# Kernel tuning notes

Measured on AMD Instinct MI355X. Metric: run time of the kernel, lower is better.

The kernel has to match this reference:

```python
import jax, jax.numpy as jnp
import numpy as np

K = 128      # knowledge_n (= net1 = prednet output width)
LOW = 64     # low_dim
PP = 64      # pp_dim
STU = 50000  # student_n
EXER = 20000 # exer_n
S_RANGES = [(0, 9999), (10000, 19999)]
NR = len(S_RANGES)
B = 4096


def setup_inputs() -> dict:
    key = jax.random.key(0)
    ks = jax.random.split(key, 16)

    def xavier(k, shape):
        fan_in, fan_out = shape[-1], shape[-2] if len(shape) > 1 else shape[-1]
        lim = np.sqrt(6.0 / (fan_in + fan_out))
        return jax.random.uniform(k, shape, jnp.float32, -lim, lim)

    return {
        "stu_id": jax.random.randint(ks[0], (B,), 0, STU),
        "exer_id": jax.random.randint(ks[1], (B,), 0, EXER),
        "kn_emb": jnp.ones((B, K), jnp.float32),
        "student_emb": xavier(ks[2], (NR, STU, LOW)),          # ParameterList stacked
        "prompt_stu": xavier(ks[3], (STU, PP)),
        "knowledge_emb": jax.random.normal(ks[4], (K, LOW), jnp.float32),
        "k_difficulty": xavier(ks[5], (EXER, LOW)),
        "s_exer_vectors": jax.random.uniform(ks[6], (NR, PP), jnp.float32),
        "W1": xavier(ks[7], (K, K + LOW)),                      # prednet_full1 (no bias)
        "W2": xavier(ks[8], (K, K + LOW)),                      # prednet_full2 (no bias)
        "W3": xavier(ks[9], (1, K)),                            # prednet_full3
        "b3": jnp.zeros((1,), jnp.float32),
        "fc1_W": xavier(ks[10], (K, PP + K)),
        "fc1_b": jnp.zeros((K,), jnp.float32),
        "fc2_W": xavier(ks[11], (K, PP + K)),
        "fc2_b": jnp.zeros((K,), jnp.float32),
    }


def reference(stu_id, exer_id, kn_emb, student_emb, prompt_stu, knowledge_emb,
              k_difficulty, s_exer_vectors, W1, W2, W3, b3, fc1_W, fc1_b, fc2_W, fc2_b):
    sig = jax.nn.sigmoid
    kle = knowledge_emb  # [K, LOW]

    # --- student side ---
    # prompt_stu.repeat(NR, 1) then index_select == index prompt_stu with stu_id % STU
    p_stu = prompt_stu[stu_id % STU]                              # [B, PP]
    stu_cat = student_emb.reshape(NR * STU, LOW)                  # concat of ParameterList
    old_stu = sig(stu_cat[stu_id] @ kle.T)                        # [B, K]
    stu_e = sig(jnp.concatenate([p_stu, old_stu], 1) @ fc1_W.T + fc1_b)  # [B, K]

    # --- exercise side ---
    counts = np.array([r[1] - r[0] + 1 for r in S_RANGES])
    temp_vectors = jnp.repeat(s_exer_vectors, counts, axis=0, total_repeat_length=EXER)
    p_exer = sig(temp_vectors[exer_id])                           # [B, PP]
    old_exer = sig(sig(k_difficulty[exer_id]) @ kle.T)            # [B, K]
    exer_e = sig(jnp.concatenate([p_exer, old_exer], 1) @ fc2_W.T + fc2_b)  # [B, K]

    # --- per-concept interaction ---
    # cat([x_broadcast, kn_vector], 2) @ W.T splits into x @ Wa.T + kle @ Wb.T
    W1a, W1b = W1[:, :K], W1[:, K:]
    W2a, W2b = W2[:, :K], W2[:, K:]
    preference = sig((stu_e @ W1a.T)[:, None, :] + (kle @ W1b.T)[None, :, :])   # [B, K, K]
    diff = sig((exer_e @ W2a.T)[:, None, :] + (kle @ W2b.T)[None, :, :])        # [B, K, K]

    o = sig((preference - diff) @ W3.T + b3)                      # [B, K, 1]
    sum_out = jnp.sum(o * kn_emb[:, :, None], axis=1)             # [B, 1]
    count = jnp.sum(kn_emb, axis=1, keepdims=True)
    return sum_out / count
```

## Files before the change

kernel.cpp:

```cpp
#include <hip/hip_runtime.h>
#include <hip/hip_bf16.h>

#define STUN   50000
#define BATCH  4096
#define LOG2E  1.4426950408889634f

__device__ __forceinline__ float fexp2(float x){ return __builtin_amdgcn_exp2f(x); }
__device__ __forceinline__ float frcp (float x){ return __builtin_amdgcn_rcpf(x); }
__device__ __forceinline__ float fsig (float x){ return frcp(1.0f + fexp2(-LOG2E * x)); }

__global__ __launch_bounds__(128) void k_pre(
    const float* __restrict__ kle,
    const float* __restrict__ W1,
    const float* __restrict__ W2,
    const float* __restrict__ fc1_W,
    const float* __restrict__ fc2_W,
    float* __restrict__ kleT,
    float* __restrict__ fc1T,
    float* __restrict__ fc2T,
    float* __restrict__ W1aT,
    float* __restrict__ W2aT,
    float* __restrict__ E1i,
    float* __restrict__ E2i)
{
    const int bid = blockIdx.x;
    const int t   = threadIdx.x;
    if (bid < 64) {
        const int u = bid;
        kleT[u * 128 + t] = kle[t * 64 + u];
    } else if (bid < 256) {
        const int u = bid - 64;
        fc1T[u * 128 + t] = fc1_W[t * 192 + u];
    } else if (bid < 448) {
        const int u = bid - 256;
        fc2T[u * 128 + t] = fc2_W[t * 192 + u];
    } else if (bid < 576) {
        const int u = bid - 448;
        W1aT[u * 128 + t] = W1[t * 192 + u];
    } else if (bid < 704) {
        const int u = bid - 576;
        W2aT[u * 128 + t] = W2[t * 192 + u];
    } else if (bid < 832) {
        const int j = bid - 704;
        float acc = 0.f;
        #pragma unroll
        for (int u4 = 0; u4 < 16; ++u4) {
            const float4 kv = *(const float4*)&kle[t * 64 + u4 * 4];
            const float4 wv = *(const float4*)&W1[j * 192 + 128 + u4 * 4];
            acc += kv.x * wv.x + kv.y * wv.y + kv.z * wv.z + kv.w * wv.w;
        }
        E1i[((j >> 2) * 128 + t) * 4 + (j & 3)] = fexp2(-LOG2E * acc);
    } else {
        const int j = bid - 832;
        float acc = 0.f;
        #pragma unroll
        for (int u4 = 0; u4 < 16; ++u4) {
            const float4 kv = *(const float4*)&kle[t * 64 + u4 * 4];
            const float4 wv = *(const float4*)&W2[j * 192 + 128 + u4 * 4];
            acc += kv.x * wv.x + kv.y * wv.y + kv.z * wv.z + kv.w * wv.w;
        }
        E2i[((j >> 2) * 128 + t) * 4 + (j & 3)] = fexp2(-LOG2E * acc);
    }
}

__global__ __launch_bounds__(256, 4) void k_fused(
    const int*   __restrict__ stu_id,
    const int*   __restrict__ exer_id,
    const float* __restrict__ student_emb,
    const float* __restrict__ prompt_stu,
    const float* __restrict__ k_diff,
    const float* __restrict__ s_exer,
    const float* __restrict__ kleT,
    const float* __restrict__ fc1T,
    const float* __restrict__ fc2T,
    const float* __restrict__ W1aT,
    const float* __restrict__ W2aT,
    const float* __restrict__ fc1_b,
    const float* __restrict__ fc2_b,
    const float* __restrict__ E1i,
    const float* __restrict__ E2i,
    const float* __restrict__ W3,
    const float* __restrict__ b3,
    const float* __restrict__ kn,
    float* __restrict__ out)
{
    __shared__ __align__(16) float sh_in [4][64][4];
    __shared__ __align__(16) float sh_old[2][128][4];
    __shared__ __align__(16) float sh_e  [2][128][4];
    __shared__ __align__(16) float ps[4][2][32][20];
    __shared__ __align__(16) float ses[2][4][128];
    __shared__ float r_o[4][2];
    __shared__ float r_k[4][2];

    const int t  = threadIdx.x;
    const int b0 = blockIdx.x * 4;

    {
        const int g   = t >> 6;
        const int u   = t & 63;
        const int sid = stu_id[b0 + g];
        const int eid = exer_id[b0 + g];
        const int er  = (eid >= 10000) ? 1 : 0;
        sh_in[0][u][g] = student_emb[sid * 64 + u];
        sh_in[1][u][g] = fsig(k_diff[eid * 64 + u]);
        sh_in[2][u][g] = prompt_stu[(sid % STUN) * 64 + u];
        sh_in[3][u][g] = fsig(s_exer[er * 64 + u]);
    }
    __syncthreads();

    const int wv   = t >> 6;
    const int l    = t & 63;
    const int half = l >> 5;
    const int iq   = l & 31;
    float* myps = &ps[wv][half][iq][0];

    const int ch   = t >> 7;
    const int cidx = t & 127;
    const int ciq  = cidx >> 2;
    const int cc   = cidx & 3;

    float a[4][4];

#define CLR { _Pragma("unroll") for (int c = 0; c < 4; ++c) \
              _Pragma("unroll") for (int b = 0; b < 4; ++b) a[c][b] = 0.f; }

#define FMAC(c, wc) { \
    a[c][0] = fmaf(wc, x0.x, a[c][0]); a[c][1] = fmaf(wc, x0.y, a[c][1]); \
    a[c][2] = fmaf(wc, x0.z, a[c][2]); a[c][3] = fmaf(wc, x0.w, a[c][3]); }

#define GSTEP(wp, xp) { \
    const float4 w4 = *(const float4*)(wp); \
    const float4 x0 = *(const float4*)&(xp)[0]; \
    FMAC(0, w4.x); FMAC(1, w4.y); FMAC(2, w4.z); FMAC(3, w4.w); }

#define PSTORE { _Pragma("unroll") for (int b = 0; b < 4; ++b) \
    *(float4*)&myps[b * 4] = make_float4(a[0][b], a[1][b], a[2][b], a[3][b]); }

#define PCOMB(res) float res[4]; \
    _Pragma("unroll") for (int b = 0; b < 4; ++b) \
        res[b] = ps[0][ch][ciq][b * 4 + cc] + ps[1][ch][ciq][b * 4 + cc] \
               + ps[2][ch][ciq][b * 4 + cc] + ps[3][ch][ciq][b * 4 + cc];

    CLR;
    {
        const int u0 = wv * 16;
        #pragma unroll 4
        for (int u = u0; u < u0 + 16; ++u)
            GSTEP(&kleT[u * 128 + iq * 4], sh_in[half][u]);
    }
    PSTORE;
    __syncthreads();
    {
        PCOMB(s);
        #pragma unroll
        for (int b = 0; b < 4; ++b) sh_old[ch][cidx][b] = fsig(s[b]);
    }
    __syncthreads();

    CLR;
    {
        const float* fcT = half ? fc2T : fc1T;
        const int u0 = wv * 48;
        const int ue_in = (u0 + 48 < 64) ? u0 + 48 : 64;
        #pragma unroll 4
        for (int u = u0; u < ue_in; ++u)
            GSTEP(&fcT[u * 128 + iq * 4], sh_in[2 + half][u]);
        const int us_old = (u0 > 64) ? u0 : 64;
        #pragma unroll 4
        for (int u = us_old; u < u0 + 48; ++u)
            GSTEP(&fcT[u * 128 + iq * 4], sh_old[half][u - 64]);
    }
    PSTORE;
    __syncthreads();
    {
        PCOMB(s);
        const float bias = (ch ? fc2_b : fc1_b)[cidx];
        #pragma unroll
        for (int b = 0; b < 4; ++b) sh_e[ch][cidx][b] = fsig(s[b] + bias);
    }
    __syncthreads();

    CLR;
    {
        const float* WT = half ? W2aT : W1aT;
        const int u0 = wv * 32;
        #pragma unroll 4
        for (int u = u0; u < u0 + 32; ++u)
            GSTEP(&WT[u * 128 + iq * 4], sh_e[half][u]);
    }
    PSTORE;
    __syncthreads();
    {
        PCOMB(s);
        #pragma unroll
        for (int b = 0; b < 4; ++b)
            ses[ch][b][cidx] = fexp2(-LOG2E * s[b]);
    }
#undef CLR
#undef FMAC
#undef GSTEP
#undef PSTORE
#undef PCOMB
    __syncthreads();

    const int k  = t & 127;
    const int bh = t >> 7;
    const int i0 = bh * 2;

    const float4* E1v = (const float4*)E1i + k;
    const float4* E2v = (const float4*)E2i + k;

    float acc0 = 0.f, acc1 = 0.f;

#define COMP(acc, esv1, esv2, e1c, e2c, w3c) { \
        const float uu = (esv1) * (e1c); \
        const float vv = (esv2) * (e2c); \
        const float dd = frcp((1.f + uu) * (1.f + vv)); \
        acc = fmaf((vv - uu) * dd, (w3c), acc); }

    #pragma unroll 4
    for (int j4 = 0; j4 < 32; ++j4) {
        const int j = j4 * 4;
        const float4 e1  = E1v[j4 * 128];
        const float4 e2  = E2v[j4 * 128];
        const float4 w3  = *(const float4*)&W3[j];
        const float4 p1a = *(const float4*)&ses[0][i0 + 0][j];
        const float4 p2a = *(const float4*)&ses[1][i0 + 0][j];
        const float4 p1b = *(const float4*)&ses[0][i0 + 1][j];
        const float4 p2b = *(const float4*)&ses[1][i0 + 1][j];
        COMP(acc0, p1a.x, p2a.x, e1.x, e2.x, w3.x);
        COMP(acc0, p1a.y, p2a.y, e1.y, e2.y, w3.y);
        COMP(acc0, p1a.z, p2a.z, e1.z, e2.z, w3.z);
        COMP(acc0, p1a.w, p2a.w, e1.w, e2.w, w3.w);
        COMP(acc1, p1b.x, p2b.x, e1.x, e2.x, w3.x);
        COMP(acc1, p1b.y, p2b.y, e1.y, e2.y, w3.y);
        COMP(acc1, p1b.z, p2b.z, e1.z, e2.z, w3.z);
        COMP(acc1, p1b.w, p2b.w, e1.w, e2.w, w3.w);
    }
#undef COMP

    const float bb3 = b3[0];
    const float o0  = fsig(acc0 + bb3);
    const float o1  = fsig(acc1 + bb3);
    const float kn0 = kn[(b0 + i0 + 0) * 128 + k];
    const float kn1 = kn[(b0 + i0 + 1) * 128 + k];
    float co0 = o0 * kn0, ck0 = kn0;
    float co1 = o1 * kn1, ck1 = kn1;
    #pragma unroll
    for (int off = 1; off < 64; off <<= 1) {
        co0 += __shfl_xor(co0, off);
        ck0 += __shfl_xor(ck0, off);
        co1 += __shfl_xor(co1, off);
        ck1 += __shfl_xor(ck1, off);
    }
    const int w = t >> 6;
    if ((t & 63) == 0) {
        r_o[w][0] = co0; r_o[w][1] = co1;
        r_k[w][0] = ck0; r_k[w][1] = ck1;
    }
    __syncthreads();
    if (t < 4) {
        const int bhh = t >> 1;
        const int i   = t & 1;
        const float so = r_o[bhh * 2][i] + r_o[bhh * 2 + 1][i];
        const float sk = r_k[bhh * 2][i] + r_k[bhh * 2 + 1][i];
        out[b0 + bhh * 2 + i] = so / sk;
    }
}

extern "C" void kernel_launch(void* const* d_in, const int* in_sizes, int n_in,
                              void* d_out, int out_size, void* d_ws, size_t ws_size,
                              hipStream_t stream)
{
    const int*   stu_id      = (const int*)  d_in[0];
    const int*   exer_id     = (const int*)  d_in[1];
    const float* kn_emb      = (const float*)d_in[2];
    const float* student_emb = (const float*)d_in[3];
    const float* prompt_stu  = (const float*)d_in[4];
    const float* kle         = (const float*)d_in[5];
    const float* k_diff      = (const float*)d_in[6];
    const float* s_exer      = (const float*)d_in[7];
    const float* W1          = (const float*)d_in[8];
    const float* W2          = (const float*)d_in[9];
    const float* W3          = (const float*)d_in[10];
    const float* b3          = (const float*)d_in[11];
    const float* fc1_W       = (const float*)d_in[12];
    const float* fc1_b       = (const float*)d_in[13];
    const float* fc2_W       = (const float*)d_in[14];
    const float* fc2_b       = (const float*)d_in[15];
    float* out = (float*)d_out;

    float* ws   = (float*)d_ws;
    float* kleT = ws;
    float* fc1T = kleT + 8192;
    float* fc2T = fc1T + 24576;
    float* W1aT = fc2T + 24576;
    float* W2aT = W1aT + 16384;
    float* E1i  = W2aT + 16384;
    float* E2i  = E1i  + 16384;

    k_pre  <<<960, 128, 0, stream>>>(kle, W1, W2, fc1_W, fc2_W,
                                     kleT, fc1T, fc2T, W1aT, W2aT, E1i, E2i);
    k_fused<<<BATCH / 4, 256, 0, stream>>>(stu_id, exer_id, student_emb, prompt_stu,
                                           k_diff, s_exer, kleT, fc1T, fc2T,
                                           W1aT, W2aT, fc1_b, fc2_b,
                                           E1i, E2i, W3, b3, kn_emb, out);
}
```

Measured before the change: 46.41 us.

## Double fused block to 512 threads and reduce GEMV partials with wave shuffles

```diff
diff --git a/kernel.cpp b/kernel.cpp
--- a/kernel.cpp
+++ b/kernel.cpp
@@ -63,7 +63,7 @@
     }
 }
 
-__global__ __launch_bounds__(256, 4) void k_fused(
+__global__ __launch_bounds__(512, 4) void k_fused(
     const int*   __restrict__ stu_id,
     const int*   __restrict__ exer_id,
     const float* __restrict__ student_emb,
@@ -87,184 +87,169 @@
     __shared__ __align__(16) float sh_in [4][64][4];
     __shared__ __align__(16) float sh_old[2][128][4];
     __shared__ __align__(16) float sh_e  [2][128][4];
-    __shared__ __align__(16) float ps[4][2][32][20];
-    __shared__ __align__(16) float ses[2][4][128];
-    __shared__ float r_o[4][2];
-    __shared__ float r_k[4][2];
+    __shared__ __align__(16) float ses   [2][4][128];
+    __shared__ float red_o[8];
+    __shared__ float red_k[8];
 
     const int t  = threadIdx.x;
     const int b0 = blockIdx.x * 4;
 
     {
-        const int g   = t >> 6;
+        const int g   = t >> 7;
+        const int sp  = (t >> 6) & 1;
         const int u   = t & 63;
         const int sid = stu_id[b0 + g];
         const int eid = exer_id[b0 + g];
-        const int er  = (eid >= 10000) ? 1 : 0;
-        sh_in[0][u][g] = student_emb[sid * 64 + u];
-        sh_in[1][u][g] = fsig(k_diff[eid * 64 + u]);
-        sh_in[2][u][g] = prompt_stu[(sid % STUN) * 64 + u];
-        sh_in[3][u][g] = fsig(s_exer[er * 64 + u]);
-    }
-    __syncthreads();
-
-    const int wv   = t >> 6;
+        if (sp == 0) {
+            sh_in[0][u][g] = student_emb[sid * 64 + u];
+            sh_in[1][u][g] = fsig(k_diff[eid * 64 + u]);
+        } else {
+            const int er = (eid >= 10000) ? 1 : 0;
+            sh_in[2][u][g] = prompt_stu[(sid % STUN) * 64 + u];
+            sh_in[3][u][g] = fsig(s_exer[er * 64 + u]);
+        }
+    }
+    __syncthreads();
+
+    const int w    = t >> 6;
+    const int half = w & 1;
+    const int iqo  = w >> 1;
     const int l    = t & 63;
-    const int half = l >> 5;
-    const int iq   = l & 31;
-    float* myps = &ps[wv][half][iq][0];
-
-    const int ch   = t >> 7;
-    const int cidx = t & 127;
-    const int ciq  = cidx >> 2;
-    const int cc   = cidx & 3;
-
-    float a[4][4];
-
-#define CLR { _Pragma("unroll") for (int c = 0; c < 4; ++c) \
-              _Pragma("unroll") for (int b = 0; b < 4; ++b) a[c][b] = 0.f; }
-
-#define FMAC(c, wc) { \
-    a[c][0] = fmaf(wc, x0.x, a[c][0]); a[c][1] = fmaf(wc, x0.y, a[c][1]); \
-    a[c][2] = fmaf(wc, x0.z, a[c][2]); a[c][3] = fmaf(wc, x0.w, a[c][3]); }
-
-#define GSTEP(wp, xp) { \
+    const int ul   = l >> 4;
+    const int bh2  = (l >> 3) & 1;
+    const int iql  = l & 7;
+    const int iq   = iqo * 8 + iql;
+
+    float a[4][2];
+
+#define CLR { _Pragma("unroll") for (int c = 0; c < 4; ++c) { a[c][0] = 0.f; a[c][1] = 0.f; } }
+
+#define GSTEP2(wp, xp) { \
     const float4 w4 = *(const float4*)(wp); \
-    const float4 x0 = *(const float4*)&(xp)[0]; \
-    FMAC(0, w4.x); FMAC(1, w4.y); FMAC(2, w4.z); FMAC(3, w4.w); }
-
-#define PSTORE { _Pragma("unroll") for (int b = 0; b < 4; ++b) \
-    *(float4*)&myps[b * 4] = make_float4(a[0][b], a[1][b], a[2][b], a[3][b]); }
-
-#define PCOMB(res) float res[4]; \
-    _Pragma("unroll") for (int b = 0; b < 4; ++b) \
-        res[b] = ps[0][ch][ciq][b * 4 + cc] + ps[1][ch][ciq][b * 4 + cc] \
-               + ps[2][ch][ciq][b * 4 + cc] + ps[3][ch][ciq][b * 4 + cc];
+    const float2 x2 = *(const float2*)(xp); \
+    a[0][0] = fmaf(w4.x, x2.x, a[0][0]); a[0][1] = fmaf(w4.x, x2.y, a[0][1]); \
+    a[1][0] = fmaf(w4.y, x2.x, a[1][0]); a[1][1] = fmaf(w4.y, x2.y, a[1][1]); \
+    a[2][0] = fmaf(w4.z, x2.x, a[2][0]); a[2][1] = fmaf(w4.z, x2.y, a[2][1]); \
+    a[3][0] = fmaf(w4.w, x2.x, a[3][0]); a[3][1] = fmaf(w4.w, x2.y, a[3][1]); }
+
+#define COMBINE { _Pragma("unroll") for (int c = 0; c < 4; ++c) { \
+    _Pragma("unroll") for (int b = 0; b < 2; ++b) { \
+        float v = a[c][b]; \
+        v += __shfl_xor(v, 16); \
+        v += __shfl_xor(v, 32); \
+        a[c][b] = v; } } }
 
     CLR;
     {
-        const int u0 = wv * 16;
-        #pragma unroll 4
+        const int u0 = ul * 16;
+        #pragma unroll
         for (int u = u0; u < u0 + 16; ++u)
-            GSTEP(&kleT[u * 128 + iq * 4], sh_in[half][u]);
-    }
-    PSTORE;
-    __syncthreads();
-    {
-        PCOMB(s);
-        #pragma unroll
-        for (int b = 0; b < 4; ++b) sh_old[ch][cidx][b] = fsig(s[b]);
+            GSTEP2(&kleT[u * 128 + iq * 4], &sh_in[half][u][bh2 * 2]);
+    }
+    COMBINE;
+    if (ul == 0) {
+        #pragma unroll
+        for (int c = 0; c < 4; ++c) {
+            const float2 v2 = make_float2(fsig(a[c][0]), fsig(a[c][1]));
+            *(float2*)&sh_old[half][iq * 4 + c][bh2 * 2] = v2;
+        }
     }
     __syncthreads();
 
     CLR;
     {
         const float* fcT = half ? fc2T : fc1T;
-        const int u0 = wv * 48;
-        const int ue_in = (u0 + 48 < 64) ? u0 + 48 : 64;
-        #pragma unroll 4
-        for (int u = u0; u < ue_in; ++u)
-            GSTEP(&fcT[u * 128 + iq * 4], sh_in[2 + half][u]);
-        const int us_old = (u0 > 64) ? u0 : 64;
-        #pragma unroll 4
-        for (int u = us_old; u < u0 + 48; ++u)
-            GSTEP(&fcT[u * 128 + iq * 4], sh_old[half][u - 64]);
-    }
-    PSTORE;
-    __syncthreads();
-    {
-        PCOMB(s);
-        const float bias = (ch ? fc2_b : fc1_b)[cidx];
-        #pragma unroll
-        for (int b = 0; b < 4; ++b) sh_e[ch][cidx][b] = fsig(s[b] + bias);
+        const int up = ul * 16;
+        #pragma unroll
+        for (int u = up; u < up + 16; ++u)
+            GSTEP2(&fcT[u * 128 + iq * 4], &sh_in[2 + half][u][bh2 * 2]);
+        const int uo = ul * 32;
+        #pragma unroll
+        for (int u = uo; u < uo + 32; ++u)
+            GSTEP2(&fcT[(64 + u) * 128 + iq * 4], &sh_old[half][u][bh2 * 2]);
+    }
+    COMBINE;
+    if (ul == 0) {
+        const float* fcb = half ? fc2_b : fc1_b;
+        #pragma unroll
+        for (int c = 0; c < 4; ++c) {
+            const float bias = fcb[iq * 4 + c];
+            const float2 v2 = make_float2(fsig(a[c][0] + bias), fsig(a[c][1] + bias));
+            *(float2*)&sh_e[half][iq * 4 + c][bh2 * 2] = v2;
+        }
     }
     __syncthreads();
 
     CLR;
     {
         const float* WT = half ? W2aT : W1aT;
-        const int u0 = wv * 32;
-        #pragma unroll 4
+        const int u0 = ul * 32;
+        #pragma unroll
         for (int u = u0; u < u0 + 32; ++u)
-            GSTEP(&WT[u * 128 + iq * 4], sh_e[half][u]);
-    }
-    PSTORE;
-    __syncthreads();
-    {
-        PCOMB(s);
-        #pragma unroll
-        for (int b = 0; b < 4; ++b)
-            ses[ch][b][cidx] = fexp2(-LOG2E * s[b]);
+            GSTEP2(&WT[u * 128 + iq * 4], &sh_e[half][u][bh2 * 2]);
+    }
+    COMBINE;
+    if (ul == 0) {
+        #pragma unroll
+        for (int c = 0; c < 4; ++c) {
+            ses[half][bh2 * 2 + 0][iq * 4 + c] = fexp2(-LOG2E * a[c][0]);
+            ses[half][bh2 * 2 + 1][iq * 4 + c] = fexp2(-LOG2E * a[c][1]);
+        }
     }
 #undef CLR
-#undef FMAC
-#undef GSTEP
-#undef PSTORE
-#undef PCOMB
+#undef GSTEP2
+#undef COMBINE
     __syncthreads();
 
     const int k  = t & 127;
     const int bh = t >> 7;
-    const int i0 = bh * 2;
 
     const float4* E1v = (const float4*)E1i + k;
     const float4* E2v = (const float4*)E2i + k;
-
-    float acc0 = 0.f, acc1 = 0.f;
-
-#define COMP(acc, esv1, esv2, e1c, e2c, w3c) { \
-        const float uu = (esv1) * (e1c); \
-        const float vv = (esv2) * (e2c); \
+    const float* s1 = &ses[0][bh][0];
+    const float* s2 = &ses[1][bh][0];
+
+    float acc = 0.f;
+
+#define COMP(s1c, s2c, e1c, e2c, w3c) { \
+        const float uu = (s1c) * (e1c); \
+        const float vv = (s2c) * (e2c); \
         const float dd = frcp((1.f + uu) * (1.f + vv)); \
         acc = fmaf((vv - uu) * dd, (w3c), acc); }
 
     #pragma unroll 4
     for (int j4 = 0; j4 < 32; ++j4) {
         const int j = j4 * 4;
-        const float4 e1  = E1v[j4 * 128];
-        const float4 e2  = E2v[j4 * 128];
-        const float4 w3  = *(const float4*)&W3[j];
-        const float4 p1a = *(const float4*)&ses[0][i0 + 0][j];
-        const float4 p2a = *(const float4*)&ses[1][i0 + 0][j];
-        const float4 p1b = *(const float4*)&ses[0][i0 + 1][j];
-        const float4 p2b = *(const float4*)&ses[1][i0 + 1][j];
-        COMP(acc0, p1a.x, p2a.x, e1.x, e2.x, w3.x);
-        COMP(acc0, p1a.y, p2a.y, e1.y, e2.y, w3.y);
-        COMP(acc0, p1a.z, p2a.z, e1.z, e2.z, w3.z);
-        COMP(acc0, p1a.w, p2a.w, e1.w, e2.w, w3.w);
-        COMP(acc1, p1b.x, p2b.x, e1.x, e2.x, w3.x);
-        COMP(acc1, p1b.y, p2b.y, e1.y, e2.y, w3.y);
-        COMP(acc1, p1b.z, p2b.z, e1.z, e2.z, w3.z);
-        COMP(acc1, p1b.w, p2b.w, e1.w, e2.w, w3.w);
+        const float4 e1 = E1v[j4 * 128];
+        const float4 e2 = E2v[j4 * 128];
+        const float4 w3 = *(const float4*)&W3[j];
+        const float4 p1 = *(const float4*)&s1[j];
+        const float4 p2 = *(const float4*)&s2[j];
+        COMP(p1.x, p2.x, e1.x, e2.x, w3.x);
+        COMP(p1.y, p2.y, e1.y, e2.y, w3.y);
+        COMP(p1.z, p2.z, e1.z, e2.z, w3.z);
+        COMP(p1.w, p2.w, e1.w, e2.w, w3.w);
     }
 #undef COMP
 
     const float bb3 = b3[0];
-    const float o0  = fsig(acc0 + bb3);
-    const float o1  = fsig(acc1 + bb3);
-    const float kn0 = kn[(b0 + i0 + 0) * 128 + k];
-    const float kn1 = kn[(b0 + i0 + 1) * 128 + k];
-    float co0 = o0 * kn0, ck0 = kn0;
-    float co1 = o1 * kn1, ck1 = kn1;
+    const float o   = fsig(acc + bb3);
+    const float knv = kn[(b0 + bh) * 128 + k];
+    float co = o * knv, ck = knv;
     #pragma unroll
     for (int off = 1; off < 64; off <<= 1) {
-        co0 += __shfl_xor(co0, off);
-        ck0 += __shfl_xor(ck0, off);
-        co1 += __shfl_xor(co1, off);
-        ck1 += __shfl_xor(ck1, off);
-    }
-    const int w = t >> 6;
+        co += __shfl_xor(co, off);
+        ck += __shfl_xor(ck, off);
+    }
     if ((t & 63) == 0) {
-        r_o[w][0] = co0; r_o[w][1] = co1;
-        r_k[w][0] = ck0; r_k[w][1] = ck1;
+        red_o[w] = co;
+        red_k[w] = ck;
     }
     __syncthreads();
     if (t < 4) {
-        const int bhh = t >> 1;
-        const int i   = t & 1;
-        const float so = r_o[bhh * 2][i] + r_o[bhh * 2 + 1][i];
-        const float sk = r_k[bhh * 2][i] + r_k[bhh * 2 + 1][i];
-        out[b0 + bhh * 2 + i] = so / sk;
+        const float so = red_o[2 * t] + red_o[2 * t + 1];
+        const float sk = red_k[2 * t] + red_k[2 * t + 1];
+        out[b0 + t] = so / sk;
     }
 }
 
@@ -301,7 +286,7 @@
 
     k_pre  <<<960, 128, 0, stream>>>(kle, W1, W2, fc1_W, fc2_W,
                                      kleT, fc1T, fc2T, W1aT, W2aT, E1i, E2i);
-    k_fused<<<BATCH / 4, 256, 0, stream>>>(stu_id, exer_id, student_emb, prompt_stu,
+    k_fused<<<BATCH / 4, 512, 0, stream>>>(stu_id, exer_id, student_emb, prompt_stu,
                                            k_diff, s_exer, kleT, fc1T, fc2T,
                                            W1aT, W2aT, fc1_b, fc2_b,
                                            E1i, E2i, W3, b3, kn_emb, out);
```

Result: slower. 55.39 us (+19.4%).

## Process eight rows per block and reduce GEMV partials with wave shuffles

Applied to the files above, without the earlier changes.

```diff
diff --git a/kernel.cpp b/kernel.cpp
--- a/kernel.cpp
+++ b/kernel.cpp
@@ -63,7 +63,7 @@
     }
 }
 
-__global__ __launch_bounds__(256, 4) void k_fused(
+__global__ __launch_bounds__(512, 4) void k_fused(
     const int*   __restrict__ stu_id,
     const int*   __restrict__ exer_id,
     const float* __restrict__ student_emb,
@@ -84,16 +84,15 @@
     const float* __restrict__ kn,
     float* __restrict__ out)
 {
-    __shared__ __align__(16) float sh_in [4][64][4];
-    __shared__ __align__(16) float sh_old[2][128][4];
-    __shared__ __align__(16) float sh_e  [2][128][4];
-    __shared__ __align__(16) float ps[4][2][32][20];
-    __shared__ __align__(16) float ses[2][4][128];
-    __shared__ float r_o[4][2];
-    __shared__ float r_k[4][2];
+    __shared__ __align__(16) float sh_in [4][64][8];
+    __shared__ __align__(16) float sh_old[2][128][8];
+    __shared__ __align__(16) float sh_e  [2][128][8];
+    __shared__ __align__(16) float ses   [2][8][128];
+    __shared__ float red_o[8][2];
+    __shared__ float red_k[8][2];
 
     const int t  = threadIdx.x;
-    const int b0 = blockIdx.x * 4;
+    const int b0 = blockIdx.x * 8;
 
     {
         const int g   = t >> 6;
@@ -108,16 +107,15 @@
     }
     __syncthreads();
 
-    const int wv   = t >> 6;
+    const int w    = t >> 6;
+    const int half = w & 1;
+    const int iqo  = w >> 1;
     const int l    = t & 63;
-    const int half = l >> 5;
-    const int iq   = l & 31;
-    float* myps = &ps[wv][half][iq][0];
-
-    const int ch   = t >> 7;
-    const int cidx = t & 127;
-    const int ciq  = cidx >> 2;
-    const int cc   = cidx & 3;
+    const int ul   = l >> 4;
+    const int bs   = (l >> 3) & 1;
+    const int iql  = l & 7;
+    const int iq   = iqo * 8 + iql;
+    const int bq   = bs * 4;
 
     float a[4][4];
 
@@ -130,77 +128,72 @@
 
 #define GSTEP(wp, xp) { \
     const float4 w4 = *(const float4*)(wp); \
-    const float4 x0 = *(const float4*)&(xp)[0]; \
+    const float4 x0 = *(const float4*)(xp); \
     FMAC(0, w4.x); FMAC(1, w4.y); FMAC(2, w4.z); FMAC(3, w4.w); }
 
-#define PSTORE { _Pragma("unroll") for (int b = 0; b < 4; ++b) \
-    *(float4*)&myps[b * 4] = make_float4(a[0][b], a[1][b], a[2][b], a[3][b]); }
-
-#define PCOMB(res) float res[4]; \
-    _Pragma("unroll") for (int b = 0; b < 4; ++b) \
-        res[b] = ps[0][ch][ciq][b * 4 + cc] + ps[1][ch][ciq][b * 4 + cc] \
-               + ps[2][ch][ciq][b * 4 + cc] + ps[3][ch][ciq][b * 4 + cc];
+#define COMBINE { _Pragma("unroll") for (int c = 0; c < 4; ++c) \
+    _Pragma("unroll") for (int b = 0; b < 4; ++b) { \
+        float v = a[c][b]; \
+        v += __shfl_xor(v, 16); \
+        v += __shfl_xor(v, 32); \
+        a[c][b] = v; } }
 
     CLR;
-    {
-        const int u0 = wv * 16;
-        #pragma unroll 4
-        for (int u = u0; u < u0 + 16; ++u)
-            GSTEP(&kleT[u * 128 + iq * 4], sh_in[half][u]);
-    }
-    PSTORE;
-    __syncthreads();
-    {
-        PCOMB(s);
-        #pragma unroll
-        for (int b = 0; b < 4; ++b) sh_old[ch][cidx][b] = fsig(s[b]);
+    #pragma unroll 4
+    for (int u = ul; u < 64; u += 4)
+        GSTEP(&kleT[u * 128 + iq * 4], &sh_in[half][u][bq]);
+    COMBINE;
+    if (ul == 0) {
+        #pragma unroll
+        for (int c = 0; c < 4; ++c)
+            *(float4*)&sh_old[half][iq * 4 + c][bq] =
+                make_float4(fsig(a[c][0]), fsig(a[c][1]), fsig(a[c][2]), fsig(a[c][3]));
     }
     __syncthreads();
 
     CLR;
     {
         const float* fcT = half ? fc2T : fc1T;
-        const int u0 = wv * 48;
-        const int ue_in = (u0 + 48 < 64) ? u0 + 48 : 64;
         #pragma unroll 4
-        for (int u = u0; u < ue_in; ++u)
-            GSTEP(&fcT[u * 128 + iq * 4], sh_in[2 + half][u]);
-        const int us_old = (u0 > 64) ? u0 : 64;
+        for (int u = ul; u < 64; u += 4)
+            GSTEP(&fcT[u * 128 + iq * 4], &sh_in[2 + half][u][bq]);
         #pragma unroll 4
-        for (int u = us_old; u < u0 + 48; ++u)
-            GSTEP(&fcT[u * 128 + iq * 4], sh_old[half][u - 64]);
-    }
-    PSTORE;
-    __syncthreads();
-    {
-        PCOMB(s);
-        const float bias = (ch ? fc2_b : fc1_b)[cidx];
-        #pragma unroll
-        for (int b = 0; b < 4; ++b) sh_e[ch][cidx][b] = fsig(s[b] + bias);
+        for (int u = 64 + ul; u < 192; u += 4)
+            GSTEP(&fcT[u * 128 + iq * 4], &sh_old[half][u - 64][bq]);
+    }
+    COMBINE;
+    if (ul == 0) {
+        const float* fcb = half ? fc2_b : fc1_b;
+        #pragma unroll
+        for (int c = 0; c < 4; ++c) {
+            const float bias = fcb[iq * 4 + c];
+            *(float4*)&sh_e[half][iq * 4 + c][bq] =
+                make_float4(fsig(a[c][0] + bias), fsig(a[c][1] + bias),
+                            fsig(a[c][2] + bias), fsig(a[c][3] + bias));
+        }
     }
     __syncthreads();
 
     CLR;
     {
         const float* WT = half ? W2aT : W1aT;
-        const int u0 = wv * 32;
         #pragma unroll 4
-        for (int u = u0; u < u0 + 32; ++u)
-            GSTEP(&WT[u * 128 + iq * 4], sh_e[half][u]);
-    }
-    PSTORE;
-    __syncthreads();
-    {
-        PCOMB(s);
-        #pragma unroll
-        for (int b = 0; b < 4; ++b)
-            ses[ch][b][cidx] = fexp2(-LOG2E * s[b]);
+        for (int u = ul; u < 128; u += 4)
+            GSTEP(&WT[u * 128 + iq * 4], &sh_e[half][u][bq]);
+    }
+    COMBINE;
+    if (ul == 0) {
+        #pragma unroll
+        for (int c = 0; c < 4; ++c) {
+            #pragma unroll
+            for (int b = 0; b < 4; ++b)
+                ses[half][bq + b][iq * 4 + c] = fexp2(-LOG2E * a[c][b]);
+        }
     }
 #undef CLR
 #undef FMAC
 #undef GSTEP
-#undef PSTORE
-#undef PCOMB
+#undef COMBINE
     __syncthreads();
 
     const int k  = t & 127;
@@ -209,25 +202,29 @@
 
     const float4* E1v = (const float4*)E1i + k;
     const float4* E2v = (const float4*)E2i + k;
+    const float* s1a = &ses[0][i0 + 0][0];
+    const float* s2a = &ses[1][i0 + 0][0];
+    const float* s1b = &ses[0][i0 + 1][0];
+    const float* s2b = &ses[1][i0 + 1][0];
 
     float acc0 = 0.f, acc1 = 0.f;
 
-#define COMP(acc, esv1, esv2, e1c, e2c, w3c) { \
-        const float uu = (esv1) * (e1c); \
-        const float vv = (esv2) * (e2c); \
+#define COMP(acc, s1c, s2c, e1c, e2c, w3c) { \
+        const float uu = (s1c) * (e1c); \
+        const float vv = (s2c) * (e2c); \
         const float dd = frcp((1.f + uu) * (1.f + vv)); \
         acc = fmaf((vv - uu) * dd, (w3c), acc); }
 
     #pragma unroll 4
     for (int j4 = 0; j4 < 32; ++j4) {
         const int j = j4 * 4;
-        const float4 e1  = E1v[j4 * 128];
-        const float4 e2  = E2v[j4 * 128];
-        const float4 w3  = *(const float4*)&W3[j];
-        const float4 p1a = *(const float4*)&ses[0][i0 + 0][j];
-        const float4 p2a = *(const float4*)&ses[1][i0 + 0][j];
-        const float4 p1b = *(const float4*)&ses[0][i0 + 1][j];
-        const float4 p2b = *(const float4*)&ses[1][i0 + 1][j];
+        const float4 e1 = E1v[j4 * 128];
+        const float4 e2 = E2v[j4 * 128];
+        const float4 w3 = *(const float4*)&W3[j];
+        const float4 p1a = *(const float4*)&s1a[j];
+        const float4 p2a = *(const float4*)&s2a[j];
+        const float4 p1b = *(const float4*)&s1b[j];
+        const float4 p2b = *(const float4*)&s2b[j];
         COMP(acc0, p1a.x, p2a.x, e1.x, e2.x, w3.x);
         COMP(acc0, p1a.y, p2a.y, e1.y, e2.y, w3.y);
         COMP(acc0, p1a.z, p2a.z, e1.z, e2.z, w3.z);
@@ -253,18 +250,17 @@
         co1 += __shfl_xor(co1, off);
         ck1 += __shfl_xor(ck1, off);
     }
-    const int w = t >> 6;
     if ((t & 63) == 0) {
-        r_o[w][0] = co0; r_o[w][1] = co1;
-        r_k[w][0] = ck0; r_k[w][1] = ck1;
-    }
-    __syncthreads();
-    if (t < 4) {
-        const int bhh = t >> 1;
-        const int i   = t & 1;
-        const float so = r_o[bhh * 2][i] + r_o[bhh * 2 + 1][i];
-        const float sk = r_k[bhh * 2][i] + r_k[bhh * 2 + 1][i];
-        out[b0 + bhh * 2 + i] = so / sk;
+        red_o[w][0] = co0; red_o[w][1] = co1;
+        red_k[w][0] = ck0; red_k[w][1] = ck1;
+    }
+    __syncthreads();
+    if (t < 8) {
+        const int p = t >> 1;
+        const int i = t & 1;
+        const float so = red_o[p * 2][i] + red_o[p * 2 + 1][i];
+        const float sk = red_k[p * 2][i] + red_k[p * 2 + 1][i];
+        out[b0 + t] = so / sk;
     }
 }
 
@@ -301,7 +297,7 @@
 
     k_pre  <<<960, 128, 0, stream>>>(kle, W1, W2, fc1_W, fc2_W,
                                      kleT, fc1T, fc2T, W1aT, W2aT, E1i, E2i);
-    k_fused<<<BATCH / 4, 256, 0, stream>>>(stu_id, exer_id, student_emb, prompt_stu,
+    k_fused<<<BATCH / 8, 512, 0, stream>>>(stu_id, exer_id, student_emb, prompt_stu,
                                            k_diff, s_exer, kleT, fc1T, fc2T,
                                            W1aT, W2aT, fc1_b, fc2_b,
                                            E1i, E2i, W3, b3, kn_emb, out);
```

Result: slower. 49.14 us (+5.9%).
